# Kernel optimization log

Hardware: AMD Instinct MI355X
Metric: run time of the kernel (lower is better)

Reference implementation:

```python
import jax, jax.numpy as jnp
import numpy as np

CUTOFFS = [16000, 28000, 36000]
HID = 1024
PROJ = [256, 64]  # hidden/4**1, hidden/4**2 per compute_proj_dims
CLUSTERS = 2


def setup_inputs() -> dict:
    key = jax.random.key(0)
    ks = jax.random.split(key, 12)
    B, S = 4, 1024
    scale = 0.02
    d = {
        "inp": jax.random.normal(ks[0], (B, S, HID), jnp.float32),
        "labels": jax.random.randint(ks[1], (B, S), 0, CUTOFFS[-1]),
        "head_W": jax.random.normal(ks[2], (HID, CUTOFFS[0] + CLUSTERS), jnp.float32) * scale,
        "head_b": jnp.zeros((CUTOFFS[0] + CLUSTERS,), jnp.float32),
    }
    for i in range(CLUSTERS):
        tdim = CUTOFFS[i + 1] - CUTOFFS[i]
        d[f"t{i}_pW"] = jax.random.normal(ks[3 + 4 * i], (HID, PROJ[i]), jnp.float32) * scale
        d[f"t{i}_pb"] = jnp.zeros((PROJ[i],), jnp.float32)
        d[f"t{i}_W"] = jax.random.normal(ks[4 + 4 * i], (PROJ[i], CUTOFFS[i + 1] - CUTOFFS[i]), jnp.float32) * scale
        d[f"t{i}_b"] = jnp.zeros((CUTOFFS[i + 1] - CUTOFFS[i],), jnp.float32)
    return d


def _sparse_ce(logits, labels):
    # stable sparse softmax cross entropy, single log_softmax pass
    logp = jax.nn.log_softmax(logits, axis=-1)
    return -jnp.take_along_axis(logp, labels[..., None], axis=-1)[..., 0]


def reference(inp, labels, head_W, head_b, t0_pW, t0_pb, t0_W, t0_b, t1_pW, t1_pb, t1_W, t1_b):
    tails = [(t0_pW, t0_pb, t0_W, t0_b), (t1_pW, t1_pb, t1_W, t1_b)]
    head_labels = labels
    loss = jnp.zeros(labels.shape, inp.dtype)
    for i, (pW, pb, W, b) in enumerate(tails):
        lo, hi = CUTOFFS[i], CUTOFFS[i + 1]
        mask = (labels >= lo) & (labels < hi)
        # tokens in cluster i are relabeled to cluster id in the head
        head_labels = jnp.where(mask, CUTOFFS[0] + i, head_labels)
        # two-layer tail projection: [B,S,H] -> [B,S,proj] -> [B,S,tail_dim]
        tail_logits = (inp @ pW + pb) @ W + b
        tail_labels = jnp.clip(labels - lo, 0, hi - lo - 1)
        loss = loss + jnp.where(mask, _sparse_ce(tail_logits, tail_labels), 0.0)
    head_logits = inp @ head_W + head_b  # [B,S,cutoffs[0]+clusters]
    loss = _sparse_ce(head_logits, head_labels) + loss
    loss = loss * (labels != 0).astype(loss.dtype)  # zero out pad positions
    return jnp.mean(loss)
```

## Files before the change

kernel.cpp:

```cpp
#include <hip/hip_runtime.h>
#include <hip/hip_bf16.h>
#include <hip/hip_fp8.h>
#include <cstdint>
#include <cstddef>

#define M_TOK 4096
#define HID   1024
#define NHEAD 16002
#define NHEAD_PAD 16384
#define P0    256
#define N0    12000
#define N0_PAD 12288
#define P1    64
#define N1    8000
#define N1_PAD 8192
#define PFUSE 384
#define PREAL 320

typedef unsigned char u8;
typedef float f32x4 __attribute__((ext_vector_type(4)));
typedef int   i32x4 __attribute__((ext_vector_type(4)));
typedef int   i32x8 __attribute__((ext_vector_type(8)));

__device__ __forceinline__ void load16(const void* g, void* l) {
    __builtin_amdgcn_global_load_lds(
        (__attribute__((address_space(1))) void*)g,
        (__attribute__((address_space(3))) void*)l,
        16, 0, 0);
}

__device__ __forceinline__ u8 to_e4m3(float f) {
    __hip_fp8_e4m3 h(f);
    return (u8)h.__x;
}

union Frag { struct { i32x4 lo, hi; } half; i32x8 v; };

struct Seg {
    const u8* A; int lda;
    const u8* BT; int ldb;
    const float* bias; int K; int realN;
    const int* tgt; float* sumexp; float* lab;
    int nblk;
};

__launch_bounds__(1024, 4)
__global__ void gemm_lse3(Seg s0, Seg s1, Seg s2) {
    __shared__ __align__(16) u8 As[2 * 32768];
    __shared__ __align__(16) u8 Bs[2 * 32768];

    int b = blockIdx.x;
    Seg sg; int rel;
    if (b < s0.nblk)                { sg = s0; rel = b; }
    else if (b < s0.nblk + s1.nblk) { sg = s1; rel = b - s0.nblk; }
    else                            { sg = s2; rel = b - s0.nblk - s1.nblk; }
    int pair = rel >> 5, inner = rel & 31;
    int m0 = (inner >> 1) * 256;
    int n0 = (pair * 2 + (inner & 1)) * 256;

    const int lda = sg.lda, ldb = sg.ldb;
    const int tid  = threadIdx.x;
    const int lane = tid & 63;
    const int wave = tid >> 6;
    const int wm = wave >> 2, wn = wave & 3;
    const int q = lane >> 4, lrow = lane & 15;
    const int sw = lrow & 7;

    int aofs[2], bofs[2], lbase[2];
    #pragma unroll
    for (int p = 0; p < 2; p++) {
        int pg = wave * 128 + p * 64 + lane;
        int row = pg >> 3, gcol = (pg & 7) ^ (row & 7);
        aofs[p]  = row * lda + gcol * 16;
        bofs[p]  = row * ldb + gcol * 16;
        lbase[p] = (wave * 128 + p * 64) * 16;
    }

    f32x4 acc[4][4];
    #pragma unroll
    for (int mt = 0; mt < 4; mt++)
        #pragma unroll
        for (int nt = 0; nt < 4; nt++)
            acc[mt][nt] = (f32x4)(0.0f);

    const u8* Ab = sg.A  + (size_t)m0 * lda;
    const u8* Bb = sg.BT + (size_t)n0 * ldb;

    const int aLo = ((wm * 64 + lrow) * 8 + ((2 * q)     ^ sw)) * 16;
    const int aHi = ((wm * 64 + lrow) * 8 + ((2 * q + 1) ^ sw)) * 16;
    const int bLo = ((wn * 64 + lrow) * 8 + ((2 * q)     ^ sw)) * 16;
    const int bHi = ((wn * 64 + lrow) * 8 + ((2 * q + 1) ^ sw)) * 16;

    auto stage = [&](int buf, int k0) {
        #pragma unroll
        for (int p = 0; p < 2; p++) {
            load16(Ab + k0 + aofs[p], As + buf * 32768 + lbase[p]);
            load16(Bb + k0 + bofs[p], Bs + buf * 32768 + lbase[p]);
        }
    };

    auto compute = [&](int buf) {
        const u8* Ac = As + buf * 32768;
        const u8* Bc = Bs + buf * 32768;
        Frag fb[4];
        #pragma unroll
        for (int t = 0; t < 4; t++) {
            fb[t].half.lo = *reinterpret_cast<const i32x4*>(Bc + bLo + t * 2048);
            fb[t].half.hi = *reinterpret_cast<const i32x4*>(Bc + bHi + t * 2048);
        }
        Frag fa[2];
        fa[0].half.lo = *reinterpret_cast<const i32x4*>(Ac + aLo);
        fa[0].half.hi = *reinterpret_cast<const i32x4*>(Ac + aHi);
        #pragma unroll
        for (int mt = 0; mt < 4; mt++) {
            if (mt < 3) {
                fa[(mt + 1) & 1].half.lo = *reinterpret_cast<const i32x4*>(Ac + aLo + (mt + 1) * 2048);
                fa[(mt + 1) & 1].half.hi = *reinterpret_cast<const i32x4*>(Ac + aHi + (mt + 1) * 2048);
            }
            #pragma unroll
            for (int nt = 0; nt < 4; nt++)
                acc[mt][nt] = __builtin_amdgcn_mfma_scale_f32_16x16x128_f8f6f4(
                    fa[mt & 1].v, fb[nt].v, acc[mt][nt],
                    0, 0,
                    0, 0x7F7F7F7F,
                    0, 0x7A7A7A7A);
        }
    };

    const int ntile = sg.K >> 7;
    stage(0, 0);
    for (int t = 0; t < ntile; ++t) {
        int cur = t & 1;
        if (t + 1 < ntile) {
            stage(cur ^ 1, (t + 1) << 7);
            asm volatile("s_waitcnt vmcnt(4)" ::: "memory");
        } else {
            asm volatile("s_waitcnt vmcnt(0)" ::: "memory");
        }
        asm volatile("s_barrier" ::: "memory");
        compute(cur);
        asm volatile("s_waitcnt lgkmcnt(0)" ::: "memory");
        asm volatile("s_barrier" ::: "memory");
    }

    int colg[4]; float bias_v[4];
    #pragma unroll
    for (int nt = 0; nt < 4; nt++) {
        colg[nt] = n0 + wn * 64 + nt * 16 + lrow;
        bias_v[nt] = (colg[nt] < sg.realN) ? sg.bias[colg[nt]] : 0.0f;
    }

    float* sred = reinterpret_cast<float*>(As);

    #pragma unroll
    for (int mt = 0; mt < 4; mt++) {
        int rloc = wm * 64 + mt * 16 + q * 4;
        #pragma unroll
        for (int r = 0; r < 4; r++) {
            int tok = m0 + rloc + r;
            int tg = sg.tgt[tok];
            float ps = 0.0f;
            #pragma unroll
            for (int nt = 0; nt < 4; nt++) {
                if (colg[nt] < sg.realN) {
                    float logit = acc[mt][nt][r] + bias_v[nt];
                    ps += __expf(logit);
                    if (colg[nt] == tg) atomicAdd(&sg.lab[tok], logit);
                }
            }
            ps += __shfl_xor(ps, 1);
            ps += __shfl_xor(ps, 2);
            ps += __shfl_xor(ps, 4);
            ps += __shfl_xor(ps, 8);
            if (lrow == 0) sred[wn * 256 + rloc + r] = ps;
        }
    }
    __syncthreads();
    if (tid < 256) {
        float v = sred[tid] + sred[256 + tid] + sred[512 + tid] + sred[768 + tid];
        atomicAdd(&sg.sumexp[m0 + tid], v);
    }
}

__launch_bounds__(512, 6)
__global__ void gemm_proj(const u8* __restrict__ A, const u8* __restrict__ BT,
                          const float* __restrict__ bias, u8* __restrict__ out) {
    __shared__ __align__(16) u8 As[16384];
    __shared__ __align__(16) u8 Bs[16384];
    const int lda = HID, ldb = HID, ldo = PFUSE;
    const int m0 = blockIdx.x * 128, n0 = blockIdx.y * 128;
    const int tid  = threadIdx.x;
    const int lane = tid & 63;
    const int wave = tid >> 6;
    const int wm = wave >> 2, wn = wave & 3;
    const int q = lane >> 4, lrow = lane & 15;
    const int sw = lrow & 7;

    int aofs[2], bofs[2], lbase[2];
    #pragma unroll
    for (int p = 0; p < 2; p++) {
        int pg = wave * 128 + p * 64 + lane;
        int row = pg >> 3, gcol = (pg & 7) ^ (row & 7);
        aofs[p]  = row * lda + gcol * 16;
        bofs[p]  = row * ldb + gcol * 16;
        lbase[p] = (wave * 128 + p * 64) * 16;
    }

    f32x4 acc[4][2];
    #pragma unroll
    for (int mt = 0; mt < 4; mt++)
        #pragma unroll
        for (int nt = 0; nt < 2; nt++)
            acc[mt][nt] = (f32x4)(0.0f);

    const u8* Ab = A  + (size_t)m0 * lda;
    const u8* Bb = BT + (size_t)n0 * ldb;

    const int aLo = ((wm * 64 + lrow) * 8 + ((2 * q)     ^ sw)) * 16;
    const int aHi = ((wm * 64 + lrow) * 8 + ((2 * q + 1) ^ sw)) * 16;
    const int bLo = ((wn * 32 + lrow) * 8 + ((2 * q)     ^ sw)) * 16;
    const int bHi = ((wn * 32 + lrow) * 8 + ((2 * q + 1) ^ sw)) * 16;

    for (int k0 = 0; k0 < HID; k0 += 128) {
        #pragma unroll
        for (int p = 0; p < 2; p++) {
            load16(Ab + k0 + aofs[p], As + lbase[p]);
            load16(Bb + k0 + bofs[p], Bs + lbase[p]);
        }
        __syncthreads();
        Frag fb[2];
        #pragma unroll
        for (int t = 0; t < 2; t++) {
            fb[t].half.lo = *reinterpret_cast<const i32x4*>(Bs + bLo + t * 2048);
            fb[t].half.hi = *reinterpret_cast<const i32x4*>(Bs + bHi + t * 2048);
        }
        #pragma unroll
        for (int mt = 0; mt < 4; mt++) {
            Frag fa;
            fa.half.lo = *reinterpret_cast<const i32x4*>(As + aLo + mt * 2048);
            fa.half.hi = *reinterpret_cast<const i32x4*>(As + aHi + mt * 2048);
            #pragma unroll
            for (int nt = 0; nt < 2; nt++)
                acc[mt][nt] = __builtin_amdgcn_mfma_scale_f32_16x16x128_f8f6f4(
                    fa.v, fb[nt].v, acc[mt][nt],
                    0, 0, 0, 0x7F7F7F7F, 0, 0x7A7A7A7A);
        }
        __syncthreads();
    }

    int colg[2]; float bias_v[2];
    #pragma unroll
    for (int nt = 0; nt < 2; nt++) {
        colg[nt] = n0 + wn * 32 + nt * 16 + lrow;
        bias_v[nt] = (colg[nt] < PREAL) ? bias[colg[nt]] : 0.0f;
    }
    #pragma unroll
    for (int mt = 0; mt < 4; mt++) {
        int rowb = m0 + wm * 64 + mt * 16 + q * 4;
        #pragma unroll
        for (int r = 0; r < 4; r++) {
            int tok = rowb + r;
            #pragma unroll
            for (int nt = 0; nt < 2; nt++)
                out[(size_t)tok * ldo + colg[nt]] = to_e4m3(acc[mt][nt][r] + bias_v[nt]);
        }
    }
}

__device__ __forceinline__ void do_transpose(const float* __restrict__ W, u8* __restrict__ WT,
                                             int K, int N, int Kpad, float scale,
                                             int bx, int by, float (*tile)[65]) {
    int n0 = bx * 64, k0 = by * 64;
    int c2 = threadIdx.x & 31;
    int rg = threadIdx.x >> 5;
    int n = n0 + c2 * 2;
    #pragma unroll
    for (int j = 0; j < 8; j++) {
        int k = k0 + rg + j * 8;
        float2 v;
        if (k < K && n + 1 < N) {
            v = *reinterpret_cast<const float2*>(&W[(size_t)k * N + n]);
        } else {
            v.x = (k < K && n     < N) ? W[(size_t)k * N + n]     : 0.0f;
            v.y = (k < K && n + 1 < N) ? W[(size_t)k * N + n + 1] : 0.0f;
        }
        tile[rg + j * 8][c2 * 2]     = v.x * scale;
        tile[rg + j * 8][c2 * 2 + 1] = v.y * scale;
    }
    __syncthreads();
    int nn = threadIdx.x >> 2, kb = (threadIdx.x & 3) * 16;
    union { u8 b[16]; uint4 u; } v;
    #pragma unroll
    for (int j = 0; j < 16; j++) v.b[j] = to_e4m3(tile[kb + j][nn]);
    *reinterpret_cast<uint4*>(WT + (size_t)(n0 + nn) * Kpad + k0 + kb) = v.u;
}

#define NBT_HEAD 4096
#define NBT_CAST 1024
#define NBT_T0W   768
#define NBT_T1W   256
#define NBT_T0P    64
#define NBT_T1P    32
#define NBT_INIT   16

__global__ void prep_kernel(const float* __restrict__ inp, const int* __restrict__ labels,
                            const float* __restrict__ head_W,
                            const float* __restrict__ t0_pW, const float* __restrict__ t0_pb,
                            const float* __restrict__ t0_W,
                            const float* __restrict__ t1_pW, const float* __restrict__ t1_pb,
                            const float* __restrict__ t1_W,
                            u8* __restrict__ inp_f8, u8* __restrict__ headW8,
                            u8* __restrict__ fpW8, u8* __restrict__ t0W8, u8* __restrict__ t1W8,
                            float* __restrict__ acc6, int* __restrict__ tgts,
                            float* __restrict__ pbias, float* __restrict__ out) {
    __shared__ float tile[64][65];
    int b = blockIdx.x;
    if (b < NBT_HEAD) {
        do_transpose(head_W, headW8, HID, NHEAD, HID, 32.0f, b % 256, b / 256, tile);
    } else if (b < NBT_HEAD + NBT_CAST) {
        int r = b - NBT_HEAD;
        int i = r * 256 + threadIdx.x;
        float4 v = reinterpret_cast<const float4*>(inp)[i];
        uchar4 o8;
        o8.x = to_e4m3(v.x); o8.y = to_e4m3(v.y); o8.z = to_e4m3(v.z); o8.w = to_e4m3(v.w);
        reinterpret_cast<uchar4*>(inp_f8)[i] = o8;
    } else if (b < NBT_HEAD + NBT_CAST + NBT_T0W) {
        int r = b - (NBT_HEAD + NBT_CAST);
        do_transpose(t0_W, t0W8, P0, N0, P0, 32.0f, r % 192, r / 192, tile);
    } else if (b < NBT_HEAD + NBT_CAST + NBT_T0W + NBT_T1W) {
        int r = b - (NBT_HEAD + NBT_CAST + NBT_T0W);
        do_transpose(t1_W, t1W8, P1, N1, 128, 32.0f, r % 128, r / 128, tile);
    } else if (b < NBT_HEAD + NBT_CAST + NBT_T0W + NBT_T1W + NBT_T0P) {
        int r = b - (NBT_HEAD + NBT_CAST + NBT_T0W + NBT_T1W);
        do_transpose(t0_pW, fpW8, HID, P0, HID, 32.0f, r % 4, r / 4, tile);
    } else if (b < NBT_HEAD + NBT_CAST + NBT_T0W + NBT_T1W + NBT_T0P + NBT_T1P) {
        int r = b - (NBT_HEAD + NBT_CAST + NBT_T0W + NBT_T1W + NBT_T0P);
        do_transpose(t1_pW, fpW8 + 256 * HID, HID, P1, HID, 32.0f, r % 2, r / 2, tile);
    } else {
        int r = b - (NBT_HEAD + NBT_CAST + NBT_T0W + NBT_T1W + NBT_T0P + NBT_T1P);
        int t = r * 256 + threadIdx.x;
        for (int j = t; j < 6 * M_TOK; j += M_TOK) acc6[j] = 0.0f;
        if (t == 0) out[0] = 0.0f;
        if (t < PFUSE) pbias[t] = (t < 256) ? t0_pb[t] : ((t < PREAL) ? t1_pb[t - 256] : 0.0f);
        int lbl = labels[t];
        tgts[t]             = (lbl < 16000) ? lbl : ((lbl < 28000) ? 16000 : 16001);
        int t0 = lbl - 16000; t0 = t0 < 0 ? 0 : (t0 > 11999 ? 11999 : t0);
        int t1 = lbl - 28000; t1 = t1 < 0 ? 0 : (t1 > 7999  ? 7999  : t1);
        tgts[M_TOK + t]     = t0;
        tgts[2 * M_TOK + t] = t1;
    }
}

__global__ void finalize_kernel(const int* __restrict__ labels, const float* __restrict__ acc6,
                                float* __restrict__ out) {
    int t = blockIdx.x * blockDim.x + threadIdx.x;
    const float* sumH = acc6;
    const float* labH = acc6 + M_TOK;
    const float* sum0 = acc6 + 2 * M_TOK;
    const float* lab0 = acc6 + 3 * M_TOK;
    const float* sum1 = acc6 + 4 * M_TOK;
    const float* lab1 = acc6 + 5 * M_TOK;
    int lbl = labels[t];
    float l = 0.0f;
    if (lbl != 0) {
        l = logf(sumH[t]) - labH[t];
        if (lbl >= 16000 && lbl < 28000) l += logf(sum0[t]) - lab0[t];
        else if (lbl >= 28000)           l += logf(sum1[t]) - lab1[t];
    }
    l *= (1.0f / (float)M_TOK);
    #pragma unroll
    for (int off = 1; off < 64; off <<= 1) l += __shfl_xor(l, off);
    __shared__ float red[4];
    if ((threadIdx.x & 63) == 0) red[threadIdx.x >> 6] = l;
    __syncthreads();
    if (threadIdx.x == 0) atomicAdd(out, red[0] + red[1] + red[2] + red[3]);
}

extern "C" void kernel_launch(void* const* d_in, const int* in_sizes, int n_in,
                              void* d_out, int out_size, void* d_ws, size_t ws_size,
                              hipStream_t stream) {
    const float* inp    = (const float*)d_in[0];
    const int*   labels = (const int*)  d_in[1];
    const float* head_W = (const float*)d_in[2];
    const float* head_b = (const float*)d_in[3];
    const float* t0_pW  = (const float*)d_in[4];
    const float* t0_pb  = (const float*)d_in[5];
    const float* t0_W   = (const float*)d_in[6];
    const float* t0_b   = (const float*)d_in[7];
    const float* t1_pW  = (const float*)d_in[8];
    const float* t1_pb  = (const float*)d_in[9];
    const float* t1_W   = (const float*)d_in[10];
    const float* t1_b   = (const float*)d_in[11];
    float* out = (float*)d_out;

    char* ws = (char*)d_ws;
    size_t off = 0;
    auto alloc = [&](size_t bytes) { char* p = ws + off; off += (bytes + 255) & ~(size_t)255; return p; };
    u8*    inp_f8  = (u8*)   alloc((size_t)M_TOK * HID);
    u8*    headW8  = (u8*)   alloc((size_t)NHEAD_PAD * HID);
    u8*    fpW8    = (u8*)   alloc((size_t)PFUSE * HID);
    u8*    t0W8    = (u8*)   alloc((size_t)N0_PAD * P0);
    u8*    t1W8    = (u8*)   alloc((size_t)N1_PAD * 128);
    u8*    proj8   = (u8*)   alloc((size_t)M_TOK * PFUSE);
    float* acc6    = (float*)alloc(6 * M_TOK * 4);
    int*   tgts    = (int*)  alloc(3 * M_TOK * 4);
    float* pbias   = (float*)alloc(PFUSE * 4);

    int nb = NBT_HEAD + NBT_CAST + NBT_T0W + NBT_T1W + NBT_T0P + NBT_T1P + NBT_INIT;
    prep_kernel<<<nb, 256, 0, stream>>>(inp, labels, head_W, t0_pW, t0_pb, t0_W,
                                        t1_pW, t1_pb, t1_W,
                                        inp_f8, headW8, fpW8, t0W8, t1W8,
                                        acc6, tgts, pbias, out);

    gemm_proj<<<dim3(M_TOK / 128, PFUSE / 128), 512, 0, stream>>>(inp_f8, fpW8, pbias, proj8);

    Seg s0{inp_f8,      HID,   headW8, HID, head_b, HID, NHEAD, tgts,             acc6,             acc6 + M_TOK,     16 * (NHEAD_PAD / 256)};
    Seg s1{proj8,       PFUSE, t0W8,   P0,  t0_b,   P0,  N0,    tgts + M_TOK,     acc6 + 2 * M_TOK, acc6 + 3 * M_TOK, 16 * (N0_PAD / 256)};
    Seg s2{proj8 + 256, PFUSE, t1W8,   128, t1_b,   128, N1,    tgts + 2 * M_TOK, acc6 + 4 * M_TOK, acc6 + 5 * M_TOK, 16 * (N1_PAD / 256)};
    gemm_lse3<<<s0.nblk + s1.nblk + s2.nblk, 1024, 0, stream>>>(s0, s1, s2);

    finalize_kernel<<<M_TOK / 256, 256, 0, stream>>>(labels, acc6, out);
}
```

Baseline: 309.6 us.

## Interleave global prefetch with MFMA phases and raise wave priority around MFMAs

Restructures the FP8 GEMM main loop into four sub-phases per K tile. Each phase issues one A-fragment LDS read and spreads the next tile's global-to-LDS loads across the first two phases. MFMA blocks are wrapped in s_setprio and sched_barrier, and barriers between phases keep waves in lockstep. The aim is to overlap memory traffic with matrix math, as in ping-pong scheduling. The cost is extra barriers per tile, and vmcnt(0) is waited only at the last phase.

```diff
diff --git a/kernel.cpp b/kernel.cpp
--- a/kernel.cpp
+++ b/kernel.cpp
@@ -91,56 +91,60 @@
     const int bLo = ((wn * 64 + lrow) * 8 + ((2 * q)     ^ sw)) * 16;
     const int bHi = ((wn * 64 + lrow) * 8 + ((2 * q + 1) ^ sw)) * 16;
 
-    auto stage = [&](int buf, int k0) {
-        #pragma unroll
-        for (int p = 0; p < 2; p++) {
-            load16(Ab + k0 + aofs[p], As + buf * 32768 + lbase[p]);
-            load16(Bb + k0 + bofs[p], Bs + buf * 32768 + lbase[p]);
-        }
-    };
-
-    auto compute = [&](int buf) {
-        const u8* Ac = As + buf * 32768;
-        const u8* Bc = Bs + buf * 32768;
-        Frag fb[4];
-        #pragma unroll
-        for (int t = 0; t < 4; t++) {
-            fb[t].half.lo = *reinterpret_cast<const i32x4*>(Bc + bLo + t * 2048);
-            fb[t].half.hi = *reinterpret_cast<const i32x4*>(Bc + bHi + t * 2048);
-        }
-        Frag fa[2];
-        fa[0].half.lo = *reinterpret_cast<const i32x4*>(Ac + aLo);
-        fa[0].half.hi = *reinterpret_cast<const i32x4*>(Ac + aHi);
-        #pragma unroll
-        for (int mt = 0; mt < 4; mt++) {
-            if (mt < 3) {
-                fa[(mt + 1) & 1].half.lo = *reinterpret_cast<const i32x4*>(Ac + aLo + (mt + 1) * 2048);
-                fa[(mt + 1) & 1].half.hi = *reinterpret_cast<const i32x4*>(Ac + aHi + (mt + 1) * 2048);
+    const int ntile = sg.K >> 7;
+    #pragma unroll
+    for (int p = 0; p < 2; p++) {
+        load16(Ab + aofs[p], As + lbase[p]);
+        load16(Bb + bofs[p], Bs + lbase[p]);
+    }
+    asm volatile("s_waitcnt vmcnt(0)" ::: "memory");
+    __builtin_amdgcn_s_barrier();
+
+    int cur = 0;
+    for (int t = 0; t < ntile; ++t, cur ^= 1) {
+        const u8* Ac = As + cur * 32768;
+        const u8* Bc = Bs + cur * 32768;
+        u8* An = As + (cur ^ 1) * 32768;
+        u8* Bn = Bs + (cur ^ 1) * 32768;
+        const bool pf = (t + 1 < ntile);
+        const int kn = (t + 1) << 7;
+
+        Frag fb[4], fa;
+        #pragma unroll
+        for (int p = 0; p < 4; ++p) {
+            if (p == 0) {
+                #pragma unroll
+                for (int i = 0; i < 4; i++) {
+                    fb[i].half.lo = *reinterpret_cast<const i32x4*>(Bc + bLo + i * 2048);
+                    fb[i].half.hi = *reinterpret_cast<const i32x4*>(Bc + bHi + i * 2048);
+                }
             }
+            fa.half.lo = *reinterpret_cast<const i32x4*>(Ac + aLo + p * 2048);
+            fa.half.hi = *reinterpret_cast<const i32x4*>(Ac + aHi + p * 2048);
+            if (pf && p == 0) {
+                load16(Ab + kn + aofs[0], An + lbase[0]);
+                load16(Ab + kn + aofs[1], An + lbase[1]);
+            }
+            if (pf && p == 1) {
+                load16(Bb + kn + bofs[0], Bn + lbase[0]);
+                load16(Bb + kn + bofs[1], Bn + lbase[1]);
+            }
+            __builtin_amdgcn_s_barrier();
+            asm volatile("s_waitcnt lgkmcnt(0)" ::: "memory");
+            __builtin_amdgcn_sched_barrier(0);
+            __builtin_amdgcn_s_setprio(1);
             #pragma unroll
             for (int nt = 0; nt < 4; nt++)
-                acc[mt][nt] = __builtin_amdgcn_mfma_scale_f32_16x16x128_f8f6f4(
-                    fa[mt & 1].v, fb[nt].v, acc[mt][nt],
+                acc[p][nt] = __builtin_amdgcn_mfma_scale_f32_16x16x128_f8f6f4(
+                    fa.v, fb[nt].v, acc[p][nt],
                     0, 0,
                     0, 0x7F7F7F7F,
                     0, 0x7A7A7A7A);
-        }
-    };
-
-    const int ntile = sg.K >> 7;
-    stage(0, 0);
-    for (int t = 0; t < ntile; ++t) {
-        int cur = t & 1;
-        if (t + 1 < ntile) {
-            stage(cur ^ 1, (t + 1) << 7);
-            asm volatile("s_waitcnt vmcnt(4)" ::: "memory");
-        } else {
-            asm volatile("s_waitcnt vmcnt(0)" ::: "memory");
-        }
-        asm volatile("s_barrier" ::: "memory");
-        compute(cur);
-        asm volatile("s_waitcnt lgkmcnt(0)" ::: "memory");
-        asm volatile("s_barrier" ::: "memory");
+            __builtin_amdgcn_s_setprio(0);
+            if (p == 3)
+                asm volatile("s_waitcnt vmcnt(0)" ::: "memory");
+            __builtin_amdgcn_s_barrier();
+        }
     }
 
     int colg[4]; float bias_v[4];
```

Measured after the change: 361.0 us. 16.6% more time.
